# Optimization experiments

Hardware: AMD Instinct MI355X
Metric: run time of the kernel (lower is better)

## Reference

```python
import jax, jax.numpy as jnp
import numpy as np
import math

HIDDEN = 1024
NUM_LAYERS = 24
INIT_RANGE = 0.02


def setup_inputs() -> dict:
    key = jax.random.key(0)
    k1, k2 = jax.random.split(key)
    B, S, H = 4, 4096, HIDDEN
    hidden_states = jax.random.normal(k1, (B, S, H), dtype=jnp.float32)
    std = INIT_RANGE / math.sqrt(2.0 * NUM_LAYERS * H)
    # queries weight: [H, H], applied as F.linear => x @ W^T
    W_q = jax.random.normal(k2, (H, H), dtype=jnp.float32) * std
    return {"hidden_states": hidden_states, "W_q": W_q}


def reference(hidden_states, W_q):
    # queries = F.linear(x, W) = x @ W^T          [B, S, H]
    q = jnp.einsum('bsh,oh->bso', hidden_states, W_q)
    # pre_attn = Q @ K^T where K = x             [B, S, S]
    pre_attn = jnp.einsum('bso,bto->bst', q, hidden_states)
    # attention = pre_attn @ V where V = x       [B, S, H]
    attention = jnp.einsum('bst,bth->bsh', pre_attn, hidden_states)
    return attention
```

## Files before the change

### kernel.cpp

```cpp
#include <hip/hip_runtime.h>
#include <hip/hip_bf16.h>
#include <stdint.h>

#define H_DIM 1024
#define S_DIM 4096
#define B_DIM 4

typedef __bf16 bf16x8 __attribute__((ext_vector_type(8)));
typedef float f32x4 __attribute__((ext_vector_type(4)));
typedef unsigned short u16x4 __attribute__((ext_vector_type(4)));

__device__ __forceinline__ unsigned short f2bf(float f) {
    union { float f; uint32_t u; } v; v.f = f;
    uint32_t u = v.u;
    uint32_t r = (u + 0x7FFFu + ((u >> 16) & 1u)) >> 16;
    return (unsigned short)r;
}
__device__ __forceinline__ float bf2f(unsigned short u) {
    union { uint32_t u; float f; } v; v.u = (uint32_t)u << 16; return v.f;
}

__device__ __forceinline__ void wg_barrier() {
    asm volatile("s_barrier" ::: "memory");
}

template <int IMM>
__device__ __forceinline__ bf16x8 ds_read_b128_imm(unsigned addr) {
    bf16x8 r;
    asm volatile("ds_read_b128 %0, %1 offset:%2"
                 : "=v"(r) : "v"(addr), "i"(IMM));
    return r;
}

__global__ void cast_x_kernel(const float* __restrict__ X,
                              unsigned short* __restrict__ Xb,
                              unsigned short* __restrict__ XT) {
    __shared__ float tile[32][33];
    const int b  = blockIdx.z;
    const int h0 = blockIdx.x * 32;
    const int s0 = blockIdx.y * 32;
    const int tx = threadIdx.x;
    const int ty = threadIdx.y;
    const float* src = X + ((size_t)b * S_DIM + s0) * H_DIM + h0;
#pragma unroll
    for (int i = 0; i < 4; ++i) {
        int s = ty + 8 * i;
        float v = src[(size_t)s * H_DIM + tx];
        tile[s][tx] = v;
        Xb[((size_t)b * S_DIM + s0 + s) * H_DIM + h0 + tx] = f2bf(v);
    }
    __syncthreads();
#pragma unroll
    for (int i = 0; i < 4; ++i) {
        int hh = ty + 8 * i;
        XT[((size_t)b * H_DIM + h0 + hh) * S_DIM + s0 + tx] = f2bf(tile[tx][hh]);
    }
}

__global__ void cast_w_kernel(const float* __restrict__ W,
                              unsigned short* __restrict__ WT) {
    __shared__ float tile[32][33];
    const int b0 = blockIdx.x * 32;
    const int o0 = blockIdx.y * 32;
    const int tx = threadIdx.x;
    const int ty = threadIdx.y;
#pragma unroll
    for (int i = 0; i < 4; ++i) {
        int o = ty + 8 * i;
        tile[o][tx] = W[(size_t)(o0 + o) * H_DIM + b0 + tx];
    }
    __syncthreads();
#pragma unroll
    for (int i = 0; i < 4; ++i) {
        int bb = ty + 8 * i;
        WT[(size_t)(b0 + bb) * H_DIM + o0 + tx] = f2bf(tile[tx][bb]);
    }
}

template <int NSPLIT>
__global__ void reduce_cast_u16_kernel(const unsigned short* __restrict__ P,
                                       unsigned short* __restrict__ Out,
                                       size_t sSplit) {
    size_t i = ((size_t)blockIdx.x * blockDim.x + threadIdx.x) * 4;
    float s0 = 0.f, s1 = 0.f, s2 = 0.f, s3 = 0.f;
#pragma unroll
    for (int sp = 0; sp < NSPLIT; ++sp) {
        u16x4 u = *(const u16x4*)&P[(size_t)sp * sSplit + i];
        s0 += bf2f(u[0]); s1 += bf2f(u[1]); s2 += bf2f(u[2]); s3 += bf2f(u[3]);
    }
    u16x4 o;
    o[0] = f2bf(s0); o[1] = f2bf(s1); o[2] = f2bf(s2); o[3] = f2bf(s3);
    *(u16x4*)&Out[i] = o;
}

template <typename OutT, int NSPLIT>
__global__ __launch_bounds__(512, 2)
void gemm_q4_kernel(const unsigned short* __restrict__ A,
                    const unsigned short* __restrict__ Bt,
                    OutT* __restrict__ C,
                    int K, int lda, int ldb, int ldc,
                    size_t sA, size_t sB, size_t sC, size_t sSplit) {
    extern __shared__ char smem_raw[];

    const int tid  = threadIdx.x;
    const int w    = tid >> 6;
    const int lane = tid & 63;
    const int wm   = w & 1;
    const int wn   = w >> 1;
    const int q    = lane >> 4;
    const int col  = lane & 15;

    const int tileM = blockIdx.x * 256;
    const int tileN = blockIdx.y * 256;
    const int bz   = blockIdx.z / NSPLIT;
    const int sp   = blockIdx.z % NSPLIT;
    const int Ksub = K / NSPLIT;
    const int T    = Ksub >> 5;

    const unsigned short* Ab = A + sA * bz + (size_t)sp * Ksub;
    const unsigned short* Bb = Bt + sB * bz + (size_t)sp * Ksub;

    auto lds3 = (__attribute__((address_space(3))) char*)&smem_raw[0];
    const unsigned ldsBase = (unsigned)(size_t)lds3;

    const unsigned aBase = ldsBase + (unsigned)(q * 4096 + wm * 2048 + col * 16);
    const unsigned bBase = ldsBase + 16384u + (unsigned)(q * 4096 + wn * 1024 + col * 16);

    const unsigned short* srcA[2];
    const unsigned short* srcB[2];
    int dstOf[2];
#pragma unroll
    for (int j = 0; j < 2; ++j) {
        int c = 2 * w + j;
        int k8l = c >> 2, r64 = c & 3;
        srcA[j] = Ab + (size_t)(tileM + r64 * 64 + lane) * lda + k8l * 8;
        srcB[j] = Bb + (size_t)(tileN + r64 * 64 + lane) * ldb + k8l * 8;
        dstOf[j] = (k8l * 256 + r64 * 64) * 16;
    }

    auto stageA = [&](int buf) {
#pragma unroll
        for (int j = 0; j < 2; ++j) {
            __builtin_amdgcn_global_load_lds(
                (const __attribute__((address_space(1))) void*)srcA[j],
                (__attribute__((address_space(3))) void*)(lds3 + buf * 32768 + dstOf[j]),
                16, 0, 0);
            srcA[j] += 32;
        }
    };
    auto stageB = [&](int buf) {
#pragma unroll
        for (int j = 0; j < 2; ++j) {
            __builtin_amdgcn_global_load_lds(
                (const __attribute__((address_space(1))) void*)srcB[j],
                (__attribute__((address_space(3))) void*)(lds3 + buf * 32768 + 16384 + dstOf[j]),
                16, 0, 0);
            srcB[j] += 32;
        }
    };

    f32x4 acc[8][4];
#pragma unroll
    for (int r = 0; r < 8; ++r)
#pragma unroll
        for (int c = 0; c < 4; ++c)
            acc[r][c] = (f32x4){0.f, 0.f, 0.f, 0.f};

    stageA(0); stageB(0);
    stageA(1); stageB(1);
    stageA(2); stageB(2);
    asm volatile("s_waitcnt vmcnt(8)" ::: "memory");
    wg_barrier();

    for (int n = 0; n < T; ++n) {
        const unsigned aAddr = aBase + (unsigned)((n & 3) << 15);
        const unsigned bAddr = bBase + (unsigned)((n & 3) << 15);
        const int nbuf = (n + 3) & 3;
        bf16x8 av[4], bv[4];

        av[0] = ds_read_b128_imm<0>(aAddr);
        av[1] = ds_read_b128_imm<256>(aAddr);
        av[2] = ds_read_b128_imm<512>(aAddr);
        av[3] = ds_read_b128_imm<768>(aAddr);
        bv[0] = ds_read_b128_imm<0>(bAddr);
        bv[1] = ds_read_b128_imm<256>(bAddr);
        bv[2] = ds_read_b128_imm<512>(bAddr);
        bv[3] = ds_read_b128_imm<768>(bAddr);
        if (n + 3 < T) stageA(nbuf);
        wg_barrier();
        asm volatile("s_waitcnt lgkmcnt(0)" ::: "memory");
        __builtin_amdgcn_sched_barrier(0);
        __builtin_amdgcn_s_setprio(1);
#pragma unroll
        for (int mf = 0; mf < 4; ++mf)
#pragma unroll
            for (int nf = 0; nf < 4; ++nf)
                acc[mf][nf] = __builtin_amdgcn_mfma_f32_16x16x32_bf16(
                    av[mf], bv[nf], acc[mf][nf], 0, 0, 0);
        __builtin_amdgcn_s_setprio(0);
        wg_barrier();

        av[0] = ds_read_b128_imm<1024>(aAddr);
        av[1] = ds_read_b128_imm<1280>(aAddr);
        av[2] = ds_read_b128_imm<1536>(aAddr);
        av[3] = ds_read_b128_imm<1792>(aAddr);
        if (n + 3 < T) stageB(nbuf);
        if (n < T - 3)       asm volatile("s_waitcnt vmcnt(8)" ::: "memory");
        else if (n == T - 3) asm volatile("s_waitcnt vmcnt(4)" ::: "memory");
        else                 asm volatile("s_waitcnt vmcnt(0)" ::: "memory");
        wg_barrier();
        asm volatile("s_waitcnt lgkmcnt(0)" ::: "memory");
        __builtin_amdgcn_sched_barrier(0);
        __builtin_amdgcn_s_setprio(1);
#pragma unroll
        for (int mf = 0; mf < 4; ++mf)
#pragma unroll
            for (int nf = 0; nf < 4; ++nf)
                acc[4 + mf][nf] = __builtin_amdgcn_mfma_f32_16x16x32_bf16(
                    av[mf], bv[nf], acc[4 + mf][nf], 0, 0, 0);
        __builtin_amdgcn_s_setprio(0);
        wg_barrier();
    }

    OutT* Cb = C + sC * bz + sSplit * sp;
    __syncthreads();
    float* lws = (float*)(smem_raw) + (size_t)w * 1088;
    const int lr = lane >> 4;
    const int lc = lane & 15;
#pragma unroll
    for (int mf = 0; mf < 8; ++mf) {
#pragma unroll
        for (int nf = 0; nf < 4; ++nf)
#pragma unroll
            for (int v = 0; v < 4; ++v)
                lws[(q * 4 + v) * 68 + nf * 16 + col] = acc[mf][nf][v];
#pragma unroll
        for (int p = 0; p < 4; ++p) {
            f32x4 t = *(const f32x4*)&lws[(p * 4 + lr) * 68 + lc * 4];
            int row  = tileM + wm * 128 + mf * 16 + p * 4 + lr;
            int colg = tileN + wn * 64 + lc * 4;
            if constexpr (sizeof(OutT) == 2) {
                u16x4 u;
                u[0] = f2bf(t[0]); u[1] = f2bf(t[1]);
                u[2] = f2bf(t[2]); u[3] = f2bf(t[3]);
                *(u16x4*)&Cb[(size_t)row * ldc + colg] = u;
            } else {
                *(f32x4*)&Cb[(size_t)row * ldc + colg] = t;
            }
        }
    }
}

extern "C" void kernel_launch(void* const* d_in, const int* in_sizes, int n_in,
                              void* d_out, int out_size, void* d_ws, size_t ws_size,
                              hipStream_t stream) {
    const float* X = (const float*)d_in[0];
    const float* W = (const float*)d_in[1];
    float* out = (float*)d_out;

    char* ws = (char*)d_ws;
    unsigned short* Xb = (unsigned short*)(ws);
    unsigned short* XT = (unsigned short*)(ws + 33554432);
    unsigned short* WT = (unsigned short*)(ws + 67108864);
    unsigned short* G  = (unsigned short*)(ws + 69206016);
    unsigned short* MT = (unsigned short*)(ws + 77594624);
    unsigned short* Gpart  = (unsigned short*)(ws + 85983232);
    unsigned short* MTpart = (unsigned short*)(ws + 85983232);

    const size_t sBH = (size_t)B_DIM * H_DIM * H_DIM;

    cast_x_kernel<<<dim3(H_DIM / 32, S_DIM / 32, B_DIM), dim3(32, 8), 0, stream>>>(X, Xb, XT);
    cast_w_kernel<<<dim3(H_DIM / 32, H_DIM / 32, 1), dim3(32, 8), 0, stream>>>(W, WT);

    gemm_q4_kernel<unsigned short, 4><<<dim3(4, 4, B_DIM * 4), 512, 131072, stream>>>(
        XT, XT, Gpart, S_DIM, S_DIM, S_DIM, H_DIM,
        (size_t)H_DIM * S_DIM, (size_t)H_DIM * S_DIM, (size_t)H_DIM * H_DIM, sBH);
    reduce_cast_u16_kernel<4><<<dim3(sBH / 4 / 256), 256, 0, stream>>>(Gpart, G, sBH);

    gemm_q4_kernel<unsigned short, 4><<<dim3(4, 4, B_DIM * 4), 512, 131072, stream>>>(
        G, WT, MTpart, H_DIM, H_DIM, H_DIM, H_DIM,
        (size_t)H_DIM * H_DIM, (size_t)0, (size_t)H_DIM * H_DIM, sBH);
    reduce_cast_u16_kernel<4><<<dim3(sBH / 4 / 256), 256, 0, stream>>>(MTpart, MT, sBH);

    gemm_q4_kernel<float, 1><<<dim3(S_DIM / 256, H_DIM / 256, B_DIM), 512, 131072, stream>>>(
        Xb, MT, out, H_DIM, H_DIM, H_DIM, H_DIM,
        (size_t)S_DIM * H_DIM, (size_t)H_DIM * H_DIM, (size_t)S_DIM * H_DIM, 0);
}
```

Before: 264.6 us.

## Cut GEMM loop to one barrier per K-step, vectorize cast and reduce kernels

The GEMM main loop now waits once per K-step, with a single vmcnt wait and barrier at the top. It then issues both A and B global-to-LDS stages for step n+3 together and reads all eight A fragments and four B fragments from LDS up front. It overlaps the second half of those LDS reads with the first MFMA block using lgkmcnt(4). This replaces the previous four barriers per step, aiming to reduce synchronisation stalls, at the cost of more live VGPRs for fragments. The x cast/transpose kernel moves to 64x64 tiles with float4 loads and 4-wide bf16 stores. The split-K reduce kernel processes 8 elements per thread with 16-byte accesses.

```diff
diff --git a/kernel.cpp b/kernel.cpp
--- a/kernel.cpp
+++ b/kernel.cpp
@@ -9,6 +9,7 @@
 typedef __bf16 bf16x8 __attribute__((ext_vector_type(8)));
 typedef float f32x4 __attribute__((ext_vector_type(4)));
 typedef unsigned short u16x4 __attribute__((ext_vector_type(4)));
+typedef unsigned short u16x8 __attribute__((ext_vector_type(8)));
 
 __device__ __forceinline__ unsigned short f2bf(float f) {
     union { float f; uint32_t u; } v; v.f = f;
@@ -32,28 +33,37 @@
     return r;
 }
 
-__global__ void cast_x_kernel(const float* __restrict__ X,
-                              unsigned short* __restrict__ Xb,
-                              unsigned short* __restrict__ XT) {
-    __shared__ float tile[32][33];
+__global__ __launch_bounds__(256)
+void cast_x_kernel(const float* __restrict__ X,
+                   unsigned short* __restrict__ Xb,
+                   unsigned short* __restrict__ XT) {
+    __shared__ float tile[64][65];
     const int b  = blockIdx.z;
-    const int h0 = blockIdx.x * 32;
-    const int s0 = blockIdx.y * 32;
+    const int h0 = blockIdx.x * 64;
+    const int s0 = blockIdx.y * 64;
     const int tx = threadIdx.x;
     const int ty = threadIdx.y;
-    const float* src = X + ((size_t)b * S_DIM + s0) * H_DIM + h0;
-#pragma unroll
-    for (int i = 0; i < 4; ++i) {
-        int s = ty + 8 * i;
-        float v = src[(size_t)s * H_DIM + tx];
-        tile[s][tx] = v;
-        Xb[((size_t)b * S_DIM + s0 + s) * H_DIM + h0 + tx] = f2bf(v);
+#pragma unroll
+    for (int j = 0; j < 4; ++j) {
+        int s = ty + 16 * j;
+        f32x4 v = *(const f32x4*)&X[((size_t)b * S_DIM + s0 + s) * H_DIM + h0 + tx * 4];
+        u16x4 o;
+#pragma unroll
+        for (int k = 0; k < 4; ++k) {
+            tile[s][tx * 4 + k] = v[k];
+            o[k] = f2bf(v[k]);
+        }
+        *(u16x4*)&Xb[((size_t)b * S_DIM + s0 + s) * H_DIM + h0 + tx * 4] = o;
     }
     __syncthreads();
 #pragma unroll
-    for (int i = 0; i < 4; ++i) {
-        int hh = ty + 8 * i;
-        XT[((size_t)b * H_DIM + h0 + hh) * S_DIM + s0 + tx] = f2bf(tile[tx][hh]);
+    for (int j = 0; j < 4; ++j) {
+        int hh = ty + 16 * j;
+        u16x4 o;
+#pragma unroll
+        for (int k = 0; k < 4; ++k)
+            o[k] = f2bf(tile[tx * 4 + k][hh]);
+        *(u16x4*)&XT[((size_t)b * H_DIM + h0 + hh) * S_DIM + s0 + tx * 4] = o;
     }
 }
 
@@ -81,16 +91,18 @@
 __global__ void reduce_cast_u16_kernel(const unsigned short* __restrict__ P,
                                        unsigned short* __restrict__ Out,
                                        size_t sSplit) {
-    size_t i = ((size_t)blockIdx.x * blockDim.x + threadIdx.x) * 4;
-    float s0 = 0.f, s1 = 0.f, s2 = 0.f, s3 = 0.f;
+    size_t i = ((size_t)blockIdx.x * blockDim.x + threadIdx.x) * 8;
+    float s[8] = {0.f, 0.f, 0.f, 0.f, 0.f, 0.f, 0.f, 0.f};
 #pragma unroll
     for (int sp = 0; sp < NSPLIT; ++sp) {
-        u16x4 u = *(const u16x4*)&P[(size_t)sp * sSplit + i];
-        s0 += bf2f(u[0]); s1 += bf2f(u[1]); s2 += bf2f(u[2]); s3 += bf2f(u[3]);
-    }
-    u16x4 o;
-    o[0] = f2bf(s0); o[1] = f2bf(s1); o[2] = f2bf(s2); o[3] = f2bf(s3);
-    *(u16x4*)&Out[i] = o;
+        u16x8 u = *(const u16x8*)&P[(size_t)sp * sSplit + i];
+#pragma unroll
+        for (int k = 0; k < 8; ++k) s[k] += bf2f(u[k]);
+    }
+    u16x8 o;
+#pragma unroll
+    for (int k = 0; k < 8; ++k) o[k] = f2bf(s[k]);
+    *(u16x8*)&Out[i] = o;
 }
 
 template <typename OutT, int NSPLIT>
@@ -169,14 +181,18 @@
     stageA(0); stageB(0);
     stageA(1); stageB(1);
     stageA(2); stageB(2);
-    asm volatile("s_waitcnt vmcnt(8)" ::: "memory");
-    wg_barrier();
 
     for (int n = 0; n < T; ++n) {
+        if (n <= T - 3)      asm volatile("s_waitcnt vmcnt(8)" ::: "memory");
+        else if (n == T - 2) asm volatile("s_waitcnt vmcnt(4)" ::: "memory");
+        else                 asm volatile("s_waitcnt vmcnt(0)" ::: "memory");
+        wg_barrier();
+
+        if (n + 3 < T) { stageA((n + 3) & 3); stageB((n + 3) & 3); }
+
         const unsigned aAddr = aBase + (unsigned)((n & 3) << 15);
         const unsigned bAddr = bBase + (unsigned)((n & 3) << 15);
-        const int nbuf = (n + 3) & 3;
-        bf16x8 av[4], bv[4];
+        bf16x8 av[8], bv[4];
 
         av[0] = ds_read_b128_imm<0>(aAddr);
         av[1] = ds_read_b128_imm<256>(aAddr);
@@ -186,9 +202,12 @@
         bv[1] = ds_read_b128_imm<256>(bAddr);
         bv[2] = ds_read_b128_imm<512>(bAddr);
         bv[3] = ds_read_b128_imm<768>(bAddr);
-        if (n + 3 < T) stageA(nbuf);
-        wg_barrier();
-        asm volatile("s_waitcnt lgkmcnt(0)" ::: "memory");
+        av[4] = ds_read_b128_imm<1024>(aAddr);
+        av[5] = ds_read_b128_imm<1280>(aAddr);
+        av[6] = ds_read_b128_imm<1536>(aAddr);
+        av[7] = ds_read_b128_imm<1792>(aAddr);
+
+        asm volatile("s_waitcnt lgkmcnt(4)" ::: "memory");
         __builtin_amdgcn_sched_barrier(0);
         __builtin_amdgcn_s_setprio(1);
 #pragma unroll
@@ -198,17 +217,7 @@
                 acc[mf][nf] = __builtin_amdgcn_mfma_f32_16x16x32_bf16(
                     av[mf], bv[nf], acc[mf][nf], 0, 0, 0);
         __builtin_amdgcn_s_setprio(0);
-        wg_barrier();
-
-        av[0] = ds_read_b128_imm<1024>(aAddr);
-        av[1] = ds_read_b128_imm<1280>(aAddr);
-        av[2] = ds_read_b128_imm<1536>(aAddr);
-        av[3] = ds_read_b128_imm<1792>(aAddr);
-        if (n + 3 < T) stageB(nbuf);
-        if (n < T - 3)       asm volatile("s_waitcnt vmcnt(8)" ::: "memory");
-        else if (n == T - 3) asm volatile("s_waitcnt vmcnt(4)" ::: "memory");
-        else                 asm volatile("s_waitcnt vmcnt(0)" ::: "memory");
-        wg_barrier();
+
         asm volatile("s_waitcnt lgkmcnt(0)" ::: "memory");
         __builtin_amdgcn_sched_barrier(0);
         __builtin_amdgcn_s_setprio(1);
@@ -217,9 +226,8 @@
 #pragma unroll
             for (int nf = 0; nf < 4; ++nf)
                 acc[4 + mf][nf] = __builtin_amdgcn_mfma_f32_16x16x32_bf16(
-                    av[mf], bv[nf], acc[4 + mf][nf], 0, 0, 0);
+                    av[4 + mf], bv[nf], acc[4 + mf][nf], 0, 0, 0);
         __builtin_amdgcn_s_setprio(0);
-        wg_barrier();
     }
 
     OutT* Cb = C + sC * bz + sSplit * sp;
@@ -269,18 +277,18 @@
 
     const size_t sBH = (size_t)B_DIM * H_DIM * H_DIM;
 
-    cast_x_kernel<<<dim3(H_DIM / 32, S_DIM / 32, B_DIM), dim3(32, 8), 0, stream>>>(X, Xb, XT);
+    cast_x_kernel<<<dim3(H_DIM / 64, S_DIM / 64, B_DIM), dim3(16, 16), 0, stream>>>(X, Xb, XT);
     cast_w_kernel<<<dim3(H_DIM / 32, H_DIM / 32, 1), dim3(32, 8), 0, stream>>>(W, WT);
 
     gemm_q4_kernel<unsigned short, 4><<<dim3(4, 4, B_DIM * 4), 512, 131072, stream>>>(
         XT, XT, Gpart, S_DIM, S_DIM, S_DIM, H_DIM,
         (size_t)H_DIM * S_DIM, (size_t)H_DIM * S_DIM, (size_t)H_DIM * H_DIM, sBH);
-    reduce_cast_u16_kernel<4><<<dim3(sBH / 4 / 256), 256, 0, stream>>>(Gpart, G, sBH);
+    reduce_cast_u16_kernel<4><<<dim3(sBH / 8 / 256), 256, 0, stream>>>(Gpart, G, sBH);
 
     gemm_q4_kernel<unsigned short, 4><<<dim3(4, 4, B_DIM * 4), 512, 131072, stream>>>(
         G, WT, MTpart, H_DIM, H_DIM, H_DIM, H_DIM,
         (size_t)H_DIM * H_DIM, (size_t)0, (size_t)H_DIM * H_DIM, sBH);
-    reduce_cast_u16_kernel<4><<<dim3(sBH / 4 / 256), 256, 0, stream>>>(MTpart, MT, sBH);
+    reduce_cast_u16_kernel<4><<<dim3(sBH / 8 / 256), 256, 0, stream>>>(MTpart, MT, sBH);
 
     gemm_q4_kernel<float, 1><<<dim3(S_DIM / 256, H_DIM / 256, B_DIM), 512, 131072, stream>>>(
         Xb, MT, out, H_DIM, H_DIM, H_DIM, H_DIM,
```

Result: no change. 262.3 us (-0.8%).
